# Kernel optimization log

Hardware: AMD Instinct MI355X
Metric: run time of the kernel (lower is better)

Reference implementation:

```python
import jax, jax.numpy as jnp
import numpy as np

INV_TEMP = 20.0
THRESHOLD = 0.01
EPS = 1e-12


def setup_inputs() -> dict:
    key = jax.random.key(0)
    k1, k2, k3, k4, k5 = jax.random.split(key, 5)
    B, NA, NB, D, K = 1, 4096, 4096, 256, 8
    return {
        "keypoints_A": jax.random.uniform(k1, (B, NA, 2), jnp.float32) * 2.0 - 1.0,
        "descriptions_A": jax.random.normal(k2, (B, NA, D), jnp.float32),
        "keypoints_B": jax.random.uniform(k3, (B, NB, 2), jnp.float32) * 2.0 - 1.0,
        "descriptions_B": jax.random.normal(k4, (B, NB, D), jnp.float32),
        # steerer prototype affine maps: one DxD matrix per prototype, scaled to
        # keep steered descriptors at unit-ish norm (acts like ~orthogonal map)
        "prototype_mats": jax.random.normal(k5, (K, D, D), jnp.float32) / np.float32(np.sqrt(D)),
    }


def _neg_dist_similarity(a, b):
    # negative Euclidean distance, matching -torch.cdist(a, b)
    a2 = jnp.sum(a * a, axis=-1)[..., :, None]   # [B, NA, 1]
    b2 = jnp.sum(b * b, axis=-1)[..., None, :]   # [B, 1, NB]
    d2 = jnp.maximum(a2 + b2 - 2.0 * jnp.einsum('bnd,bmd->bnm', a, b), 0.0)
    return -jnp.sqrt(d2 + EPS)                   # [B, NA, NB]


def reference(keypoints_A, descriptions_A, keypoints_B, descriptions_B, prototype_mats):
    # base similarity
    corr = _neg_dist_similarity(descriptions_A, descriptions_B)  # [B, NA, NB]

    # looped augmented-similarity max-accumulate (one pass per prototype affine)
    def step(c, M):
        dA_aug = jnp.einsum('bnd,ed->bne', descriptions_A, M)  # steered descriptors
        return jnp.maximum(c, _neg_dist_similarity(dA_aug, descriptions_B)), None

    corr, _ = jax.lax.scan(step, corr, prototype_mats)

    corr = INV_TEMP * corr
    # dual softmax matching
    P = jax.nn.softmax(corr, axis=-2) * jax.nn.softmax(corr, axis=-1)  # [B, NA, NB]

    # mutual nearest neighbour + threshold (fixed-shape boolean mask instead of nonzero)
    mask = (P == P.max(axis=-1, keepdims=True)) \
         & (P == P.max(axis=-2, keepdims=True)) \
         & (P > THRESHOLD)

    # fixed-shape match extraction: best B-index per A keypoint + validity flag
    j = jnp.argmax(P, axis=-1)                                   # [B, NA]
    valid = jnp.take_along_axis(mask, j[..., None], axis=-1)[..., 0]  # [B, NA]
    matches_B = jnp.take_along_axis(keypoints_B, j[..., None], axis=1)  # [B, NA, 2]
    return P, mask, valid, matches_B
```

## Files before the change

### kernel.cpp

```cpp
#include <hip/hip_runtime.h>
#include <math.h>

#define NPT 4096
#define DIM 256
#define NVAR 9
#define INV_TEMP 20.0f
#define THR 0.01f
#define EPSD 1e-12f

typedef unsigned short u16;
typedef __attribute__((ext_vector_type(8))) __bf16 bf16x8;
typedef __attribute__((ext_vector_type(4))) float f32x4;

__device__ __forceinline__ unsigned frep(float x) {
    unsigned u = __float_as_uint(x);
    return (u & 0x80000000u) ? ~u : (u | 0x80000000u);
}
__device__ __forceinline__ float funrep(unsigned u) {
    return __uint_as_float((u & 0x80000000u) ? (u ^ 0x80000000u) : ~u);
}

__device__ __forceinline__ u16 f2bf(float x) {
    unsigned u = __float_as_uint(x);
    u += 0x7fffu + ((u >> 16) & 1u);
    return (u16)(u >> 16);
}
__device__ __forceinline__ float bf2f(u16 h) {
    return __uint_as_float(((unsigned)h) << 16);
}
__device__ __forceinline__ void split_hl(float x, u16& h, u16& l) {
    u16 hh = f2bf(x);
    h = hh;
    l = f2bf(x - bf2f(hh));
}

__device__ __forceinline__ void gl_lds16(const void* g, void* l) {
    __builtin_amdgcn_global_load_lds(
        (const __attribute__((address_space(1))) void*)g,
        (__attribute__((address_space(3))) void*)l, 16, 0, 0);
}

#define NA4 (NPT * DIM / 4)
#define NP4 (8 * DIM * DIM / 4)
__global__ __launch_bounds__(256) void conv3_kernel(const float* __restrict__ A,
                                                    const float* __restrict__ B,
                                                    const float* __restrict__ Pr,
                                                    u16* __restrict__ Ahi, u16* __restrict__ Alo,
                                                    u16* __restrict__ Bhi, u16* __restrict__ Blo,
                                                    u16* __restrict__ Phi, u16* __restrict__ Plo) {
    int i = blockIdx.x * 256 + threadIdx.x;
    const float* src;
    u16 *dh, *dl;
    int j;
    if (i < NA4) { src = A; dh = Ahi; dl = Alo; j = i; }
    else if (i < 2 * NA4) { src = B; dh = Bhi; dl = Blo; j = i - NA4; }
    else if (i < 2 * NA4 + NP4) { src = Pr; dh = Phi; dl = Plo; j = i - 2 * NA4; }
    else return;
    float4 v = ((const float4*)src)[j];
    ushort4 h, l;
    split_hl(v.x, h.x, l.x);
    split_hl(v.y, h.y, l.y);
    split_hl(v.z, h.z, l.z);
    split_hl(v.w, h.w, l.w);
    ((ushort4*)dh)[j] = h;
    ((ushort4*)dl)[j] = l;
}

__global__ __launch_bounds__(256, 2) void steer_mfma_kernel(
    const u16* __restrict__ A0h, const u16* __restrict__ A0l,
    const u16* __restrict__ Ph, const u16* __restrict__ Pl,
    u16* __restrict__ outH, u16* __restrict__ outL) {
    __shared__ u16 lds[32768];
    u16* LAh = lds;
    u16* LAl = lds + 8192;
    u16* LBh = lds + 16384;
    u16* LBl = lds + 24576;

    const int tid = threadIdx.x, lane = tid & 63, wave = tid >> 6;
    const int l15 = lane & 15, lg = lane >> 4;
    const int wr = (wave >> 1) * 64, wc = (wave & 1) * 64;
    const int rb = blockIdx.x * 128;
    const int eb = blockIdx.y * 128;
    const int k = blockIdx.z;
    const u16* Bh_g = Ph + (size_t)k * DIM * DIM;
    const u16* Bl_g = Pl + (size_t)k * DIM * DIM;
    const int s_row = tid >> 3;
    const int s_ch = tid & 7;
    const int s_gch = s_ch ^ (s_row & 7);
    const int c0 = lg ^ (l15 & 7);

    f32x4 acc[4][4];
#pragma unroll
    for (int m = 0; m < 4; ++m)
#pragma unroll
        for (int n = 0; n < 4; ++n) acc[m][n] = 0.0f;

    for (int kb = 0; kb < 4; ++kb) {
        const int k0 = kb * 64;
        __syncthreads();
#pragma unroll
        for (int r = 0; r < 4; ++r) {
            int row = r * 32 + s_row;
            size_t ga = (size_t)(rb + row) * DIM + k0 + s_gch * 8;
            size_t gb = (size_t)(eb + row) * DIM + k0 + s_gch * 8;
            int lo = row * 64 + s_ch * 8;
            gl_lds16(A0h + ga, &LAh[lo]);
            gl_lds16(A0l + ga, &LAl[lo]);
            gl_lds16(Bh_g + gb, &LBh[lo]);
            gl_lds16(Bl_g + gb, &LBl[lo]);
        }
        __syncthreads();
#pragma unroll
        for (int ks = 0; ks < 2; ++ks) {
            const int cx = (c0 ^ (ks << 2)) * 8;
            bf16x8 ah[4], al[4], bh[4], bl[4];
#pragma unroll
            for (int m = 0; m < 4; ++m) {
                int ro = (wr + m * 16 + l15) * 64 + cx;
                ah[m] = *(const bf16x8*)&LAh[ro];
                al[m] = *(const bf16x8*)&LAl[ro];
            }
#pragma unroll
            for (int n = 0; n < 4; ++n) {
                int ro = (wc + n * 16 + l15) * 64 + cx;
                bh[n] = *(const bf16x8*)&LBh[ro];
                bl[n] = *(const bf16x8*)&LBl[ro];
            }
#pragma unroll
            for (int m = 0; m < 4; ++m)
#pragma unroll
                for (int n = 0; n < 4; ++n)
                    acc[m][n] = __builtin_amdgcn_mfma_f32_16x16x32_bf16(ah[m], bh[n], acc[m][n], 0, 0, 0);
#pragma unroll
            for (int m = 0; m < 4; ++m)
#pragma unroll
                for (int n = 0; n < 4; ++n)
                    acc[m][n] = __builtin_amdgcn_mfma_f32_16x16x32_bf16(al[m], bh[n], acc[m][n], 0, 0, 0);
#pragma unroll
            for (int m = 0; m < 4; ++m)
#pragma unroll
                for (int n = 0; n < 4; ++n)
                    acc[m][n] = __builtin_amdgcn_mfma_f32_16x16x32_bf16(ah[m], bl[n], acc[m][n], 0, 0, 0);
        }
    }
#pragma unroll
    for (int m = 0; m < 4; ++m)
#pragma unroll
        for (int j = 0; j < 4; ++j) {
            size_t row = (size_t)(k + 1) * NPT + rb + wr + m * 16 + lg * 4 + j;
#pragma unroll
            for (int n = 0; n < 4; ++n) {
                u16 h, l;
                split_hl(acc[m][n][j], h, l);
                size_t idx = row * DIM + eb + wc + n * 16 + l15;
                outH[idx] = h;
                outL[idx] = l;
            }
        }
}

__global__ __launch_bounds__(256) void rownorm10_kernel(const u16* __restrict__ AH,
                                                        const u16* __restrict__ AL,
                                                        const u16* __restrict__ BH,
                                                        const u16* __restrict__ BL,
                                                        float* __restrict__ out) {
    int w = blockIdx.x * 4 + (threadIdx.x >> 6);
    int lane = threadIdx.x & 63;
    const u16 *H, *L;
    size_t row;
    if (w < NVAR * NPT) { H = AH; L = AL; row = w; }
    else { H = BH; L = BL; row = w - NVAR * NPT; }
    ushort4 h = *(const ushort4*)&H[row * DIM + lane * 4];
    ushort4 l = *(const ushort4*)&L[row * DIM + lane * 4];
    float x0 = bf2f(h.x) + bf2f(l.x);
    float x1 = bf2f(h.y) + bf2f(l.y);
    float x2 = bf2f(h.z) + bf2f(l.z);
    float x3 = bf2f(h.w) + bf2f(l.w);
    float s = x0 * x0 + x1 * x1 + x2 * x2 + x3 * x3;
#pragma unroll
    for (int o = 32; o; o >>= 1) s += __shfl_xor(s, o);
    if (lane == 0) out[w] = s;
}

__global__ __launch_bounds__(256, 2) void corr_mfma_kernel(
    const u16* __restrict__ Ahi, const u16* __restrict__ Alo,
    const u16* __restrict__ Bhi, const u16* __restrict__ Blo,
    const float* __restrict__ a2, const float* __restrict__ b2,
    float* __restrict__ cOut, unsigned* __restrict__ rm_rep, unsigned* __restrict__ cm_rep,
    float* __restrict__ pMaxR, float* __restrict__ pSumR,
    float* __restrict__ pMaxC, float* __restrict__ pSumC) {
    __shared__ u16 lds[32768];
    u16* LAh = lds;
    u16* LAl = lds + 8192;
    u16* LBh = lds + 16384;
    u16* LBl = lds + 24576;

    const int tid = threadIdx.x, lane = tid & 63, wave = tid >> 6;
    const int l15 = lane & 15, lg = lane >> 4;
    const int wr = (wave >> 1) * 64, wc = (wave & 1) * 64;
    int wg = blockIdx.y * 32 + blockIdx.x;
    wg = (wg & 7) * 128 + (wg >> 3);
    const int rb = (wg >> 5) * 128;
    const int cb = (wg & 31) * 128;
    const int rbIdx = rb >> 7, cbIdx = cb >> 7;
    const int s_row = tid >> 3;
    const int s_ch = tid & 7;
    const int s_gch = s_ch ^ (s_row & 7);
    const int c0 = lg ^ (l15 & 7);

    float b2c[4];
#pragma unroll
    for (int n = 0; n < 4; ++n) b2c[n] = b2[cb + wc + n * 16 + l15];

    f32x4 zmin[4][4];
#pragma unroll
    for (int m = 0; m < 4; ++m)
#pragma unroll
        for (int n = 0; n < 4; ++n) zmin[m][n] = 3.402823466e38f;

    for (int v = 0; v < NVAR; ++v) {
        const u16* Ah_g = Ahi + (size_t)v * NPT * DIM;
        const u16* Al_g = Alo + (size_t)v * NPT * DIM;
        f32x4 acc[4][4];
#pragma unroll
        for (int m = 0; m < 4; ++m)
#pragma unroll
            for (int n = 0; n < 4; ++n) acc[m][n] = 0.0f;

        for (int kb = 0; kb < 4; ++kb) {
            const int k0 = kb * 64;
            __syncthreads();
#pragma unroll
            for (int r = 0; r < 4; ++r) {
                int row = r * 32 + s_row;
                size_t ga = (size_t)(rb + row) * DIM + k0 + s_gch * 8;
                size_t gb = (size_t)(cb + row) * DIM + k0 + s_gch * 8;
                int lo = row * 64 + s_ch * 8;
                gl_lds16(Ah_g + ga, &LAh[lo]);
                gl_lds16(Al_g + ga, &LAl[lo]);
                gl_lds16(Bhi + gb, &LBh[lo]);
                gl_lds16(Blo + gb, &LBl[lo]);
            }
            __syncthreads();
#pragma unroll
            for (int ks = 0; ks < 2; ++ks) {
                const int cx = (c0 ^ (ks << 2)) * 8;
                bf16x8 ah[4], al[4], bh[4], bl[4];
#pragma unroll
                for (int m = 0; m < 4; ++m) {
                    int ro = (wr + m * 16 + l15) * 64 + cx;
                    ah[m] = *(const bf16x8*)&LAh[ro];
                    al[m] = *(const bf16x8*)&LAl[ro];
                }
#pragma unroll
                for (int n = 0; n < 4; ++n) {
                    int ro = (wc + n * 16 + l15) * 64 + cx;
                    bh[n] = *(const bf16x8*)&LBh[ro];
                    bl[n] = *(const bf16x8*)&LBl[ro];
                }
#pragma unroll
                for (int m = 0; m < 4; ++m)
#pragma unroll
                    for (int n = 0; n < 4; ++n)
                        acc[m][n] = __builtin_amdgcn_mfma_f32_16x16x32_bf16(ah[m], bh[n], acc[m][n], 0, 0, 0);
#pragma unroll
                for (int m = 0; m < 4; ++m)
#pragma unroll
                    for (int n = 0; n < 4; ++n)
                        acc[m][n] = __builtin_amdgcn_mfma_f32_16x16x32_bf16(al[m], bh[n], acc[m][n], 0, 0, 0);
#pragma unroll
                for (int m = 0; m < 4; ++m)
#pragma unroll
                    for (int n = 0; n < 4; ++n)
                        acc[m][n] = __builtin_amdgcn_mfma_f32_16x16x32_bf16(ah[m], bl[n], acc[m][n], 0, 0, 0);
            }
        }
#pragma unroll
        for (int m = 0; m < 4; ++m) {
            float4 a4 = *(const float4*)&a2[(size_t)v * NPT + rb + wr + m * 16 + lg * 4];
            const float* a4p = (const float*)&a4;
#pragma unroll
            for (int n = 0; n < 4; ++n)
#pragma unroll
                for (int j = 0; j < 4; ++j) {
                    float d2 = fmaxf(a4p[j] + b2c[n] - 2.0f * acc[m][n][j], 0.0f);
                    zmin[m][n][j] = fminf(zmin[m][n][j], d2);
                }
        }
    }

    unsigned* redR = (unsigned*)lds;
    unsigned* redC = redR + 128;
    float* bsumR = (float*)(redC + 128);
    float* bsumC = bsumR + 128;
    __syncthreads();
    if (tid < 128) { redR[tid] = 0u; redC[tid] = 0u; bsumR[tid] = 0.f; bsumC[tid] = 0.f; }
    __syncthreads();

    float colmax[4] = {-3.402823466e38f, -3.402823466e38f, -3.402823466e38f, -3.402823466e38f};
#pragma unroll
    for (int m = 0; m < 4; ++m) {
#pragma unroll
        for (int j = 0; j < 4; ++j) {
            int row = rb + wr + m * 16 + lg * 4 + j;
            float rmax = -3.402823466e38f;
#pragma unroll
            for (int n = 0; n < 4; ++n) {
                float c = -INV_TEMP * sqrtf(zmin[m][n][j] + EPSD);
                cOut[(size_t)row * NPT + cb + wc + n * 16 + l15] = c;
                rmax = fmaxf(rmax, c);
                colmax[n] = fmaxf(colmax[n], c);
            }
            atomicMax(&redR[wr + m * 16 + lg * 4 + j], frep(rmax));
        }
    }
#pragma unroll
    for (int n = 0; n < 4; ++n)
        atomicMax(&redC[wc + n * 16 + l15], frep(colmax[n]));
    __syncthreads();

    float bmc[4], colS[4];
#pragma unroll
    for (int n = 0; n < 4; ++n) {
        bmc[n] = funrep(redC[wc + n * 16 + l15]);
        colS[n] = 0.f;
    }
#pragma unroll
    for (int m = 0; m < 4; ++m) {
#pragma unroll
        for (int j = 0; j < 4; ++j) {
            int lr = wr + m * 16 + lg * 4 + j;
            float bm = funrep(redR[lr]);
            float s = 0.f;
#pragma unroll
            for (int n = 0; n < 4; ++n) {
                float c = -INV_TEMP * sqrtf(zmin[m][n][j] + EPSD);
                s += __expf(c - bm);
                colS[n] += __expf(c - bmc[n]);
            }
            s += __shfl_xor(s, 1);
            s += __shfl_xor(s, 2);
            s += __shfl_xor(s, 4);
            s += __shfl_xor(s, 8);
            if (l15 == 0) atomicAdd(&bsumR[lr], s);
        }
    }
#pragma unroll
    for (int n = 0; n < 4; ++n) {
        float s = colS[n];
        s += __shfl_xor(s, 16);
        s += __shfl_xor(s, 32);
        if (lg == 0) atomicAdd(&bsumC[wc + n * 16 + l15], s);
    }
    __syncthreads();

    if (tid < 128) {
        atomicMax(&rm_rep[rb + tid], redR[tid]);
        pMaxR[(size_t)cbIdx * NPT + rb + tid] = funrep(redR[tid]);
        pSumR[(size_t)cbIdx * NPT + rb + tid] = bsumR[tid];
    } else {
        int t = tid - 128;
        atomicMax(&cm_rep[cb + t], redC[t]);
        pMaxC[(size_t)rbIdx * NPT + cb + t] = funrep(redC[t]);
        pSumC[(size_t)rbIdx * NPT + cb + t] = bsumC[t];
    }
}

__global__ __launch_bounds__(256) void combine_kernel(const unsigned* __restrict__ rm_rep,
                                                      const unsigned* __restrict__ cm_rep,
                                                      const float* __restrict__ pMaxR,
                                                      const float* __restrict__ pSumR,
                                                      const float* __restrict__ pMaxC,
                                                      const float* __restrict__ pSumC,
                                                      float* __restrict__ rowsum,
                                                      float* __restrict__ colsum) {
    int idx = (blockIdx.x & 15) * 256 + threadIdx.x;
    if (blockIdx.x < 16) {
        float gm = funrep(rm_rep[idx]);
        float s = 0.f;
#pragma unroll
        for (int b = 0; b < 32; ++b)
            s += pSumR[(size_t)b * NPT + idx] * __expf(pMaxR[(size_t)b * NPT + idx] - gm);
        rowsum[idx] = s;
    } else {
        float gm = funrep(cm_rep[idx]);
        float s = 0.f;
#pragma unroll
        for (int b = 0; b < 32; ++b)
            s += pSumC[(size_t)b * NPT + idx] * __expf(pMaxC[(size_t)b * NPT + idx] - gm);
        colsum[idx] = s;
    }
}


__global__ __launch_bounds__(256) void pmax_kernel(float* __restrict__ C,
                                                   const unsigned* __restrict__ rm_rep,
                                                   const unsigned* __restrict__ cm_rep,
                                                   const float* __restrict__ rowsum,
                                                   const float* __restrict__ colsum,
                                                   unsigned* __restrict__ rmp_rep,
                                                   unsigned* __restrict__ cmp_rep) {
    const int tid = threadIdx.x, lane = tid & 63, wv = tid >> 6;
    const int c0 = (blockIdx.x & 15) * 256;
    const int r0 = (blockIdx.x >> 4) * 64;
    const int colq = (c0 >> 2) + lane;
    __shared__ float rmbuf[64], rrbuf[64];
    __shared__ float pmLds[64 * 65];
    __shared__ float qred[256];
    __shared__ float cred[4][256];
    if (tid < 64) {
        rmbuf[tid] = funrep(rm_rep[r0 + tid]);
        rrbuf[tid] = 1.0f / rowsum[r0 + tid];
    }
    uint4 cmr = ((const uint4*)cm_rep)[colq];
    float cm0 = funrep(cmr.x), cm1 = funrep(cmr.y), cm2 = funrep(cmr.z), cm3 = funrep(cmr.w);
    float4 csv = ((const float4*)colsum)[colq];
    float rc0 = 1.0f / csv.x, rc1 = 1.0f / csv.y, rc2 = 1.0f / csv.z, rc3 = 1.0f / csv.w;
    __syncthreads();
    float4 cmax = make_float4(-1.f, -1.f, -1.f, -1.f);
#pragma unroll
    for (int it = 0; it < 16; ++it) {
        int lr = it * 4 + wv;
        int r = r0 + lr;
        size_t idx = (size_t)r * (NPT / 4) + colq;
        float4 cv = ((const float4*)C)[idx];
        float rm = rmbuf[lr];
        float rr = rrbuf[lr];
        float4 p;
        p.x = __expf(2.0f * cv.x - cm0 - rm) * (rc0 * rr);
        p.y = __expf(2.0f * cv.y - cm1 - rm) * (rc1 * rr);
        p.z = __expf(2.0f * cv.z - cm2 - rm) * (rc2 * rr);
        p.w = __expf(2.0f * cv.w - cm3 - rm) * (rc3 * rr);
        ((float4*)C)[idx] = p;
        pmLds[lr * 65 + lane] = fmaxf(fmaxf(p.x, p.y), fmaxf(p.z, p.w));
        cmax.x = fmaxf(cmax.x, p.x);
        cmax.y = fmaxf(cmax.y, p.y);
        cmax.z = fmaxf(cmax.z, p.z);
        cmax.w = fmaxf(cmax.w, p.w);
    }
    cred[wv][lane * 4 + 0] = cmax.x;
    cred[wv][lane * 4 + 1] = cmax.y;
    cred[wv][lane * 4 + 2] = cmax.z;
    cred[wv][lane * 4 + 3] = cmax.w;
    __syncthreads();
    {
        int row = tid & 63, q = tid >> 6;
        float m = -1.f;
#pragma unroll
        for (int i = 0; i < 16; ++i) m = fmaxf(m, pmLds[row * 65 + q * 16 + i]);
        qred[row * 4 + q] = m;
    }
    float mc = fmaxf(fmaxf(cred[0][tid], cred[1][tid]), fmaxf(cred[2][tid], cred[3][tid]));
    atomicMax(&cmp_rep[c0 + tid], frep(mc));
    __syncthreads();
    if (tid < 64) {
        float m = fmaxf(fmaxf(qred[tid * 4 + 0], qred[tid * 4 + 1]),
                        fmaxf(qred[tid * 4 + 2], qred[tid * 4 + 3]));
        atomicMax(&rmp_rep[r0 + tid], frep(m));
    }
}

__global__ __launch_bounds__(256) void maskarg_kernel(const float* __restrict__ P,
                                                      const unsigned* __restrict__ rmp_rep,
                                                      const unsigned* __restrict__ cmp_rep,
                                                      float* __restrict__ maskOut,
                                                      int* __restrict__ argJ) {
    const int tid = threadIdx.x, lane = tid & 63, wv = tid >> 6;
    const int c0 = (blockIdx.x & 15) * 256;
    const int r0 = (blockIdx.x >> 4) * 64;
    const int colq = (c0 >> 2) + lane;
    const int col4 = c0 + lane * 4;
    __shared__ float rpbuf[64];
    __shared__ int candLds[64 * 65];
    __shared__ int qredi[256];
    if (tid < 64) rpbuf[tid] = funrep(rmp_rep[r0 + tid]);
    uint4 cpr = ((const uint4*)cmp_rep)[colq];
    float cp0 = funrep(cpr.x), cp1 = funrep(cpr.y), cp2 = funrep(cpr.z), cp3 = funrep(cpr.w);
    __syncthreads();
#pragma unroll
    for (int it = 0; it < 16; ++it) {
        int lr = it * 4 + wv;
        int r = r0 + lr;
        size_t idx = (size_t)r * (NPT / 4) + colq;
        float4 p = ((const float4*)P)[idx];
        float rmp = rpbuf[lr];
        float4 m;
        m.x = (p.x == rmp && p.x == cp0 && p.x > THR) ? 1.f : 0.f;
        m.y = (p.y == rmp && p.y == cp1 && p.y > THR) ? 1.f : 0.f;
        m.z = (p.z == rmp && p.z == cp2 && p.z > THR) ? 1.f : 0.f;
        m.w = (p.w == rmp && p.w == cp3 && p.w > THR) ? 1.f : 0.f;
        ((float4*)maskOut)[idx] = m;
        int cand = 0x7fffffff;
        if (p.w == rmp) cand = col4 + 3;
        if (p.z == rmp) cand = col4 + 2;
        if (p.y == rmp) cand = col4 + 1;
        if (p.x == rmp) cand = col4 + 0;
        candLds[lr * 65 + lane] = cand;
    }
    __syncthreads();
    {
        int row = tid & 63, q = tid >> 6;
        int m = 0x7fffffff;
#pragma unroll
        for (int i = 0; i < 16; ++i) m = min(m, candLds[row * 65 + q * 16 + i]);
        qredi[row * 4 + q] = m;
    }
    __syncthreads();
    if (tid < 64) {
        int m = min(min(qredi[tid * 4 + 0], qredi[tid * 4 + 1]),
                    min(qredi[tid * 4 + 2], qredi[tid * 4 + 3]));
        atomicMin(&argJ[r0 + tid], m);
    }
}

__global__ __launch_bounds__(256) void valid_kernel(const float* __restrict__ P,
                                                    const unsigned* __restrict__ cmp_rep,
                                                    const int* __restrict__ argJ,
                                                    const float* __restrict__ kpB,
                                                    float* __restrict__ validOut,
                                                    float* __restrict__ matchOut) {
    int n = blockIdx.x * 256 + threadIdx.x;
    int j = argJ[n];
    float pj = P[(size_t)n * NPT + j];
    bool v = (pj == funrep(cmp_rep[j])) && (pj > THR);
    validOut[n] = v ? 1.f : 0.f;
    matchOut[2 * n + 0] = kpB[2 * j + 0];
    matchOut[2 * n + 1] = kpB[2 * j + 1];
}

extern "C" void kernel_launch(void* const* d_in, const int* in_sizes, int n_in,
                              void* d_out, int out_size, void* d_ws, size_t ws_size,
                              hipStream_t stream) {
    const float* dA     = (const float*)d_in[1];
    const float* kpB    = (const float*)d_in[2];
    const float* dB     = (const float*)d_in[3];
    const float* protos = (const float*)d_in[4];

    float* P      = (float*)d_out;
    float* maskO  = P + (size_t)NPT * NPT;
    float* validO = maskO + (size_t)NPT * NPT;
    float* matchO = validO + NPT;

    u16* Ahi = (u16*)maskO;
    u16* Alo = Ahi + (size_t)NVAR * NPT * DIM;
    u16* Bhi = Alo + (size_t)NVAR * NPT * DIM;
    u16* Blo = Bhi + (size_t)NPT * DIM;
    u16* Phi = Blo + (size_t)NPT * DIM;
    u16* Plo = Phi + (size_t)8 * DIM * DIM;
    float* pMaxR = (float*)(Plo + (size_t)8 * DIM * DIM);
    float* pSumR = pMaxR + 32 * NPT;
    float* pMaxC = pSumR + 32 * NPT;
    float* pSumC = pMaxC + 32 * NPT;

    float* ws      = (float*)d_ws;
    float* a2      = ws;
    float* b2      = a2 + NVAR * NPT;
    unsigned* rm   = (unsigned*)(b2 + NPT);
    unsigned* cm   = rm + NPT;
    unsigned* rmp  = cm + NPT;
    unsigned* cmp  = rmp + NPT;
    float* rs      = (float*)(cmp + NPT);
    float* cs      = rs + NPT;
    int* argJ      = (int*)(cs + NPT);

    hipMemsetAsync(rm, 0, 4 * NPT * sizeof(unsigned), stream);
    hipMemsetAsync(argJ, 0x7f, NPT * sizeof(int), stream);

    conv3_kernel<<<2560, 256, 0, stream>>>(dA, dB, protos, Ahi, Alo, Bhi, Blo, Phi, Plo);
    steer_mfma_kernel<<<dim3(32, 2, 8), 256, 0, stream>>>(Ahi, Alo, Phi, Plo, Ahi, Alo);
    rownorm10_kernel<<<(NVAR + 1) * NPT / 4, 256, 0, stream>>>(Ahi, Alo, Bhi, Blo, a2);
    corr_mfma_kernel<<<dim3(32, 32), 256, 0, stream>>>(Ahi, Alo, Bhi, Blo, a2, b2, P, rm, cm,
                                                       pMaxR, pSumR, pMaxC, pSumC);
    combine_kernel<<<32, 256, 0, stream>>>(rm, cm, pMaxR, pSumR, pMaxC, pSumC, rs, cs);
    pmax_kernel<<<1024, 256, 0, stream>>>(P, rm, cm, rs, cs, rmp, cmp);
    maskarg_kernel<<<1024, 256, 0, stream>>>(P, rmp, cmp, maskO, argJ);
    valid_kernel<<<16, 256, 0, stream>>>(P, cmp, argJ, kpB, validO, matchO);
}
```

Before: 408.9 us.

## Fuse steered-descriptor row norms into steer GEMM epilogue and remap corr tiles per XCD

The steer GEMM epilogue now accumulates squared norms of the steered descriptors in fp32 and adds them into a2 with atomics. The separate row-norm pass therefore only handles the base A and B descriptors, which avoids re-reading 8×4096 rows of hi/lo bf16 data. The norm uses the fp32 accumulator instead of the hi+lo reconstruction, so results can differ slightly, and an extra memset is needed. The corr kernel's workgroup-to-tile mapping is also changed so each XCD covers a contiguous 8x16 block of tiles, aiming for better L2 locality.

```diff
diff --git a/kernel.cpp b/kernel.cpp
--- a/kernel.cpp
+++ b/kernel.cpp
@@ -69,7 +69,8 @@
 __global__ __launch_bounds__(256, 2) void steer_mfma_kernel(
     const u16* __restrict__ A0h, const u16* __restrict__ A0l,
     const u16* __restrict__ Ph, const u16* __restrict__ Pl,
-    u16* __restrict__ outH, u16* __restrict__ outL) {
+    u16* __restrict__ outH, u16* __restrict__ outL,
+    float* __restrict__ a2out) {
     __shared__ u16 lds[32768];
     u16* LAh = lds;
     u16* LAl = lds + 8192;
@@ -148,28 +149,37 @@
 #pragma unroll
         for (int j = 0; j < 4; ++j) {
             size_t row = (size_t)(k + 1) * NPT + rb + wr + m * 16 + lg * 4 + j;
+            float s2 = 0.f;
 #pragma unroll
             for (int n = 0; n < 4; ++n) {
+                float s = acc[m][n][j];
+                s2 += s * s;
                 u16 h, l;
-                split_hl(acc[m][n][j], h, l);
+                split_hl(s, h, l);
                 size_t idx = row * DIM + eb + wc + n * 16 + l15;
                 outH[idx] = h;
                 outL[idx] = l;
             }
-        }
-}
-
-__global__ __launch_bounds__(256) void rownorm10_kernel(const u16* __restrict__ AH,
-                                                        const u16* __restrict__ AL,
-                                                        const u16* __restrict__ BH,
-                                                        const u16* __restrict__ BL,
-                                                        float* __restrict__ out) {
+            s2 += __shfl_xor(s2, 1);
+            s2 += __shfl_xor(s2, 2);
+            s2 += __shfl_xor(s2, 4);
+            s2 += __shfl_xor(s2, 8);
+            if (l15 == 0) atomicAdd(&a2out[row], s2);
+        }
+}
+
+__global__ __launch_bounds__(256) void rownorm2_kernel(const u16* __restrict__ AH,
+                                                       const u16* __restrict__ AL,
+                                                       const u16* __restrict__ BH,
+                                                       const u16* __restrict__ BL,
+                                                       float* __restrict__ out) {
     int w = blockIdx.x * 4 + (threadIdx.x >> 6);
     int lane = threadIdx.x & 63;
     const u16 *H, *L;
     size_t row;
-    if (w < NVAR * NPT) { H = AH; L = AL; row = w; }
-    else { H = BH; L = BL; row = w - NVAR * NPT; }
+    int oidx;
+    if (w < NPT) { H = AH; L = AL; row = w; oidx = w; }
+    else { H = BH; L = BL; row = w - NPT; oidx = NVAR * NPT + (w - NPT); }
     ushort4 h = *(const ushort4*)&H[row * DIM + lane * 4];
     ushort4 l = *(const ushort4*)&L[row * DIM + lane * 4];
     float x0 = bf2f(h.x) + bf2f(l.x);
@@ -179,7 +189,7 @@
     float s = x0 * x0 + x1 * x1 + x2 * x2 + x3 * x3;
 #pragma unroll
     for (int o = 32; o; o >>= 1) s += __shfl_xor(s, o);
-    if (lane == 0) out[w] = s;
+    if (lane == 0) out[oidx] = s;
 }
 
 __global__ __launch_bounds__(256, 2) void corr_mfma_kernel(
@@ -199,10 +209,11 @@
     const int l15 = lane & 15, lg = lane >> 4;
     const int wr = (wave >> 1) * 64, wc = (wave & 1) * 64;
     int wg = blockIdx.y * 32 + blockIdx.x;
-    wg = (wg & 7) * 128 + (wg >> 3);
-    const int rb = (wg >> 5) * 128;
-    const int cb = (wg & 31) * 128;
-    const int rbIdx = rb >> 7, cbIdx = cb >> 7;
+    const int xcd = wg & 7, idx8 = wg >> 3;
+    const int rbIdx = ((xcd >> 1) << 3) + (idx8 >> 4);
+    const int cbIdx = ((xcd & 1) << 4) + (idx8 & 15);
+    const int rb = rbIdx << 7;
+    const int cb = cbIdx << 7;
     const int s_row = tid >> 3;
     const int s_ch = tid & 7;
     const int s_gch = s_ch ^ (s_row & 7);
@@ -563,12 +574,13 @@
     float* cs      = rs + NPT;
     int* argJ      = (int*)(cs + NPT);
 
+    hipMemsetAsync(a2 + NPT, 0, 8 * NPT * sizeof(float), stream);
     hipMemsetAsync(rm, 0, 4 * NPT * sizeof(unsigned), stream);
     hipMemsetAsync(argJ, 0x7f, NPT * sizeof(int), stream);
 
     conv3_kernel<<<2560, 256, 0, stream>>>(dA, dB, protos, Ahi, Alo, Bhi, Blo, Phi, Plo);
-    steer_mfma_kernel<<<dim3(32, 2, 8), 256, 0, stream>>>(Ahi, Alo, Phi, Plo, Ahi, Alo);
-    rownorm10_kernel<<<(NVAR + 1) * NPT / 4, 256, 0, stream>>>(Ahi, Alo, Bhi, Blo, a2);
+    steer_mfma_kernel<<<dim3(32, 2, 8), 256, 0, stream>>>(Ahi, Alo, Phi, Plo, Ahi, Alo, a2);
+    rownorm2_kernel<<<2 * NPT / 4, 256, 0, stream>>>(Ahi, Alo, Bhi, Blo, a2);
     corr_mfma_kernel<<<dim3(32, 32), 256, 0, stream>>>(Ahi, Alo, Bhi, Blo, a2, b2, P, rm, cm,
                                                        pMaxR, pSumR, pMaxC, pSumC);
     combine_kernel<<<32, 256, 0, stream>>>(rm, cm, pMaxR, pSumR, pMaxC, pSumC, rs, cs);
```

Measured after the change: 424.6 us. 1.04x slower.
